# Kernel tuning notes

Measured on AMD Instinct MI355X. Metric: run time of the kernel, lower is better.

## Reference

```python
import math
import jax, jax.numpy as jnp
import numpy as np

B, T, D, H = 2, 2048, 1024, 16
N_LAYERS = 24


def get_slopes(n):
    def pow2(n):
        start = 2 ** (-2 ** (-(math.log2(n) - 3)))
        return [start * start ** i for i in range(n)]
    if math.log2(n).is_integer():
        return pow2(n)
    c = 2 ** math.floor(math.log2(n))
    return pow2(c) + get_slopes(2 * c)[0::2][: n - c]


def setup_inputs() -> dict:
    key = jax.random.key(0)
    ks = jax.random.split(key, 5)
    x = jax.random.normal(ks[0], (B, T, D), dtype=jnp.float32)
    Wq = 0.02 * jax.random.normal(ks[1], (D, D), dtype=jnp.float32)
    Wk = 0.02 * jax.random.normal(ks[2], (D, D), dtype=jnp.float32)
    Wv = 0.02 * jax.random.normal(ks[3], (D, D), dtype=jnp.float32)
    Wo = (0.02 / math.sqrt(2 * N_LAYERS)) * jax.random.normal(ks[4], (D, D), dtype=jnp.float32)
    z = jnp.zeros((D,), dtype=jnp.float32)
    return {"x": x, "Wq": Wq, "bq": z, "Wk": Wk, "bk": z, "Wv": Wv, "bv": z, "Wo": Wo, "bo": z}


def reference(x, Wq, bq, Wk, bk, Wv, bv, Wo, bo):
    Bb, Tt, C = x.shape
    hd = C // H
    # QKV projections -> (B, H, T, hd)
    q = (x @ Wq + bq).reshape(Bb, Tt, H, hd).transpose(0, 2, 1, 3)
    k = (x @ Wk + bk).reshape(Bb, Tt, H, hd).transpose(0, 2, 1, 3)
    v = (x @ Wv + bv).reshape(Bb, Tt, H, hd).transpose(0, 2, 1, 3)
    # scaled dot-product scores (B, H, T, T)
    attn = jnp.einsum('bhqd,bhkd->bhqk', q, k) / jnp.sqrt(jnp.asarray(hd, x.dtype))
    # ALiBi bias: module uses only last row of the relative-position matrix,
    # broadcast over query positions: -slope_h * (T-1 - j), shape (1, H, 1, T)
    slopes = jnp.asarray(get_slopes(H), dtype=x.dtype)
    alibi = -slopes[None, :, None, None] * (Tt - 1 - jnp.arange(Tt, dtype=x.dtype))[None, None, None, :]
    attn = attn + alibi
    # causal mask
    causal = jnp.tril(jnp.ones((Tt, Tt), dtype=bool))[None, None, :, :]
    attn = jnp.where(causal, attn, jnp.finfo(x.dtype).min)
    p = jax.nn.softmax(attn, axis=-1)
    out = jnp.einsum('bhqk,bhkd->bqhd', p, v).reshape(Bb, Tt, C)
    return out @ Wo + bo
```

## Files before the change

kernel.cpp:

```cpp
#include <hip/hip_runtime.h>
#include <hip/hip_bf16.h>

#define Bn 2
#define Tdim 2048
#define Ddim 1024
#define Hn 16
#define HD 64

typedef unsigned short u16;
typedef unsigned int u32;
typedef __attribute__((ext_vector_type(8))) __bf16 bf16x8;
typedef __attribute__((ext_vector_type(4))) float f32x4;
typedef __attribute__((ext_vector_type(16))) float f32x16;
typedef __attribute__((ext_vector_type(4))) u32 u32x4;

struct alignas(8) U16x4 { u16 x, y, z, w; };

__device__ __forceinline__ u16 f2bf(float f) {
  union { float f; u32 i; } v; v.f = f;
  u32 x = v.i;
  u32 r = (x + 0x7fffu + ((x >> 16) & 1u)) >> 16;
  return (u16)r;
}
__device__ __forceinline__ float bf2f(u16 u) {
  union { u32 i; float f; } v; v.i = ((u32)u) << 16; return v.f;
}
__device__ __forceinline__ u32 fbits(float f) {
  union { float f; u32 i; } v; v.f = f; return v.i;
}

__device__ __forceinline__ void cp16(const u16* g, u16* l) {
  __builtin_amdgcn_global_load_lds(
      (const __attribute__((address_space(1))) u32*)g,
      (__attribute__((address_space(3))) u32*)l, 16, 0, 0);
}

__device__ __forceinline__ f32x4 mfma16(bf16x8 a, bf16x8 b, f32x4 c) {
  return __builtin_amdgcn_mfma_f32_16x16x32_bf16(a, b, c, 0, 0, 0);
}
__device__ __forceinline__ f32x16 mfma32(bf16x8 a, bf16x8 b, f32x16 c) {
  return __builtin_amdgcn_mfma_f32_32x32x16_bf16(a, b, c, 0, 0, 0);
}

__global__ __launch_bounds__(256) void convert_x(const float* __restrict__ src,
                                                 u16* __restrict__ dst) {
  const int i = (blockIdx.x * 256 + threadIdx.x) * 8;
  u16 t[8];
#pragma unroll
  for (int j = 0; j < 8; j++) t[j] = f2bf(src[i + j]);
  *(bf16x8*)&dst[i] = *(const bf16x8*)t;
}

__global__ __launch_bounds__(256) void transpose_k(
    const float* __restrict__ s0, const float* __restrict__ s1,
    const float* __restrict__ s2, const float* __restrict__ s3,
    u16* __restrict__ dst) {
  const float* src = (blockIdx.z == 0) ? s0 : (blockIdx.z == 1) ? s1
                   : (blockIdx.z == 2) ? s2 : s3;
  u16* d = dst + (size_t)blockIdx.z * Ddim * Ddim;
  __shared__ u16 tile[32][33];
  const int tx = threadIdx.x, ty = threadIdx.y;
  const int x = blockIdx.x * 32 + tx;
  const int y0 = blockIdx.y * 32;
#pragma unroll
  for (int j = 0; j < 32; j += 8) tile[ty + j][tx] = f2bf(src[(size_t)(y0 + ty + j) * Ddim + x]);
  __syncthreads();
  const int xo = blockIdx.y * 32 + tx;
  const int yo0 = blockIdx.x * 32;
#pragma unroll
  for (int j = 0; j < 32; j += 8) d[(size_t)(yo0 + ty + j) * Ddim + xo] = tile[tx][ty + j];
}

__global__ __launch_bounds__(256, 2) void gemm_qkv(
    const u16* __restrict__ Xb, const u16* __restrict__ WT,
    const float* __restrict__ bq, const float* __restrict__ bk, const float* __restrict__ bv,
    u16* __restrict__ Q, u16* __restrict__ K, u16* __restrict__ Vt) {
  const int z = blockIdx.z;
  const u16* Wt = WT + (size_t)z * Ddim * Ddim;
  const float* bias = (z == 0) ? bq : (z == 1) ? bk : bv;
  u16* QK = (z == 0) ? Q : K;

  __shared__ alignas(16) u16 Alds[128 * 32];
  __shared__ alignas(16) u16 Blds[128 * 32];
  const int tid = threadIdx.x;
  const int w = tid >> 6, lane = tid & 63, ln = lane & 15, quad = lane >> 4;
  const int wm = (w >> 1) * 64, wn = (w & 1) * 64;
  const int tm = blockIdx.x * 128, tn = blockIdx.y * 128;

  f32x4 acc[4][4] = {};

  const int srow = tid >> 2, scol = (tid & 3) * 8;
  const u16* ag = Xb + (size_t)(tm + srow) * Ddim + scol;
  const u16* ag2 = ag + (size_t)64 * Ddim;
  const u16* bg = Wt + (size_t)(tn + srow) * Ddim + scol;
  const u16* bg2 = bg + (size_t)64 * Ddim;
  u16* al = &Alds[w * 512];
  u16* al2 = &Alds[2048 + w * 512];
  u16* bl = &Blds[w * 512];
  u16* bl2 = &Blds[2048 + w * 512];

  for (int k0 = 0; k0 < Ddim; k0 += 32) {
    __syncthreads();
    cp16(ag + k0, al);
    cp16(ag2 + k0, al2);
    cp16(bg + k0, bl);
    cp16(bg2 + k0, bl2);
    __syncthreads();
    bf16x8 af[4], bfr[4];
#pragma unroll
    for (int i = 0; i < 4; i++)
      af[i] = *(const bf16x8*)&Alds[(wm + i * 16 + ln) * 32 + quad * 8];
#pragma unroll
    for (int i = 0; i < 4; i++)
      bfr[i] = *(const bf16x8*)&Blds[(wn + i * 16 + ln) * 32 + quad * 8];
#pragma unroll
    for (int mi = 0; mi < 4; mi++)
#pragma unroll
      for (int ni = 0; ni < 4; ni++)
        acc[mi][ni] = mfma16(af[mi], bfr[ni], acc[mi][ni]);
  }

#pragma unroll
  for (int mi = 0; mi < 4; mi++) {
#pragma unroll
    for (int ni = 0; ni < 4; ni++) {
      const int gm0 = tm + wm + mi * 16 + quad * 4;
      const int gn = tn + wn + ni * 16 + ln;
      const float bv_ = bias[gn];
      const int hh = gn >> 6, dd = gn & 63;
      const int b0 = gm0 >> 11, t0 = gm0 & 2047;
      if (z < 2) {
        u16* p = QK + (((size_t)(b0 * Hn + hh) * Tdim) + t0) * HD + dd;
#pragma unroll
        for (int r = 0; r < 4; r++) p[r * HD] = f2bf(acc[mi][ni][r] + bv_);
      } else {
        U16x4 pk;
        pk.x = f2bf(acc[mi][ni][0] + bv_);
        pk.y = f2bf(acc[mi][ni][1] + bv_);
        pk.z = f2bf(acc[mi][ni][2] + bv_);
        pk.w = f2bf(acc[mi][ni][3] + bv_);
        *(U16x4*)&Vt[((size_t)(b0 * Hn + hh) * HD + dd) * Tdim + t0] = pk;
      }
    }
  }
}

#define KSTR 68
#define VSTR 132
#define L2E 1.44269504088896f
__global__ __launch_bounds__(256, 2) void attn_k(
    const u16* __restrict__ Q, const u16* __restrict__ K, const u16* __restrict__ Vt,
    u16* __restrict__ Op, float* __restrict__ lp) {
  __shared__ alignas(16) u16 Klds[128 * KSTR];
  __shared__ alignas(16) u16 Vtlds[64 * VSTR];

  const int bx = blockIdx.x;
  const int qb = 15 - (bx >> 1);
  const int s = bx & 1;
  const int bh = blockIdx.y;
  const int q0 = qb * 128;
  const int tid = threadIdx.x;
  const int w = tid >> 6, lane = tid & 63;
  const int qi = lane & 31, hf = lane >> 5;

  const u16* Qh = Q + (size_t)bh * Tdim * HD;
  const u16* Kh = K + (size_t)bh * Tdim * HD;
  const u16* Vh = Vt + (size_t)bh * HD * Tdim;
  const float slope = exp2f(-0.5f * (float)((bh & 15) + 1));

  const int nkt = qb + 1;
  const int h0 = (nkt + 1) >> 1;
  const int kt0 = s ? h0 : 0;
  const int kt1 = s ? nkt : h0;

  const int tg = q0 + w * 32 + qi;
  const float sl2 = slope * L2E;
  const float c1 = 0.125f * L2E;
  const float tt2 = (slope * (float)tg + 3.0f) * L2E;
  const float f4hf = (float)(4 * hf);
  float sg8[4], slm[4];
#pragma unroll
  for (int g = 0; g < 4; g++) sg8[g] = sl2 * (float)(8 * g);
#pragma unroll
  for (int m = 0; m < 4; m++) slm[m] = sl2 * (float)m;

  bf16x8 qf[4];
#pragma unroll
  for (int kc = 0; kc < 4; kc++)
    qf[kc] = *(const bf16x8*)&Qh[(size_t)tg * HD + kc * 16 + hf * 8];

  float lsum = 0.f;
  f32x16 oacc[2] = {};

  bf16x8 kreg[4], vreg[4];
  {
    const int kb = kt0 * 128;
#pragma unroll
    for (int c = 0; c < 4; c++) {
      const int e = c * 2048 + tid * 8;
      kreg[c] = *(const bf16x8*)&Kh[(size_t)(kb + (e >> 6)) * HD + (e & 63)];
      vreg[c] = *(const bf16x8*)&Vh[(size_t)(e >> 7) * Tdim + kb + (e & 127)];
    }
  }

  for (int kt = kt0; kt < kt1; kt++) {
    const int kb = kt * 128;
    __syncthreads();
#pragma unroll
    for (int c = 0; c < 4; c++) {
      const int e = c * 2048 + tid * 8;
      *(bf16x8*)&Klds[(e >> 6) * KSTR + (e & 63)] = kreg[c];
      *(bf16x8*)&Vtlds[(e >> 7) * VSTR + (e & 127)] = vreg[c];
    }
    __syncthreads();

    if (kt + 1 < kt1) {
      const int kb2 = kb + 128;
#pragma unroll
      for (int c = 0; c < 4; c++) {
        const int e = c * 2048 + tid * 8;
        kreg[c] = *(const bf16x8*)&Kh[(size_t)(kb2 + (e >> 6)) * HD + (e & 63)];
        vreg[c] = *(const bf16x8*)&Vh[(size_t)(e >> 7) * Tdim + kb2 + (e & 127)];
      }
    }

    f32x16 st[4] = {};
#pragma unroll
    for (int kc = 0; kc < 4; kc++) {
#pragma unroll
      for (int ni = 0; ni < 4; ni++) {
        bf16x8 kf = *(const bf16x8*)&Klds[(ni * 32 + qi) * KSTR + kc * 16 + hf * 8];
        st[ni] = mfma32(kf, qf[kc], st[ni]);
      }
    }

    const bool diag = (kt == nkt - 1);
    const float fkb = (float)kb + f4hf;
    bf16x8 pfrag[8];
#pragma unroll
    for (int ni = 0; ni < 4; ni++) {
      const float cni = __builtin_fmaf(sl2, fkb + (float)(32 * ni), -tt2);
      u32 pu[16];
      if (!diag) {
#pragma unroll
        for (int ri = 0; ri < 16; ri++) {
          const float e = __builtin_fmaf(st[ni][ri], c1, cni + sg8[ri >> 2] + slm[ri & 3]);
          const float p = __builtin_amdgcn_exp2f(e);
          lsum += p;
          pu[ri] = fbits(p) + 0x8000u;
        }
      } else {
#pragma unroll
        for (int ri = 0; ri < 16; ri++) {
          const int n = kb + ni * 32 + (ri & 3) + 8 * (ri >> 2) + 4 * hf;
          const float e = __builtin_fmaf(st[ni][ri], c1, cni + sg8[ri >> 2] + slm[ri & 3]);
          float p = __builtin_amdgcn_exp2f(e);
          if (n > tg) p = 0.f;
          lsum += p;
          pu[ri] = fbits(p) + 0x8000u;
        }
      }
      u32 pk[4][2];
#pragma unroll
      for (int g = 0; g < 4; g++) {
        pk[g][0] = __builtin_amdgcn_perm(pu[g * 4 + 1], pu[g * 4 + 0], 0x07060302u);
        pk[g][1] = __builtin_amdgcn_perm(pu[g * 4 + 3], pu[g * 4 + 2], 0x07060302u);
      }
#pragma unroll
      for (int a = 0; a < 2; a++) {
        const u32 snd0 = (hf == 0) ? pk[2 * a + 1][0] : pk[2 * a][0];
        const u32 snd1 = (hf == 0) ? pk[2 * a + 1][1] : pk[2 * a][1];
        const u32 rcv0 = (u32)__shfl_xor((int)snd0, 32);
        const u32 rcv1 = (u32)__shfl_xor((int)snd1, 32);
        u32x4 fr;
        fr.x = (hf == 0) ? pk[2 * a][0] : rcv0;
        fr.y = (hf == 0) ? pk[2 * a][1] : rcv1;
        fr.z = (hf == 0) ? rcv0 : pk[2 * a + 1][0];
        fr.w = (hf == 0) ? rcv1 : pk[2 * a + 1][1];
        pfrag[ni * 2 + a] = *(bf16x8*)&fr;
      }
    }

#pragma unroll
    for (int kf16 = 0; kf16 < 8; kf16++) {
#pragma unroll
      for (int nd = 0; nd < 2; nd++) {
        bf16x8 vf = *(const bf16x8*)&Vtlds[(nd * 32 + qi) * VSTR + kf16 * 16 + hf * 8];
        oacc[nd] = mfma32(pfrag[kf16], vf, oacc[nd]);
      }
    }
  }

  lsum += __shfl_xor(lsum, 32);
  if (hf == 0) lp[(size_t)s * 65536 + bh * Tdim + tg] = lsum;

  u16* Ob = Op + (size_t)s * (32u * Tdim * HD) + ((size_t)bh * Tdim) * HD;
#pragma unroll
  for (int nd = 0; nd < 2; nd++) {
#pragma unroll
    for (int ri = 0; ri < 16; ri++) {
      const int rq = (ri & 3) + 8 * (ri >> 2) + 4 * hf;
      const int t = q0 + w * 32 + rq;
      Ob[(size_t)t * HD + nd * 32 + qi] = f2bf(oacc[nd][ri]);
    }
  }
}

__global__ __launch_bounds__(256) void merge_k(const u16* __restrict__ Op,
                                               const float* __restrict__ lp,
                                               u16* __restrict__ AO) {
  const int i = blockIdx.x * 256 + threadIdx.x;
  const int d8 = i & 7;
  const int t = (i >> 3) & 2047;
  const int bh = i >> 14;
  const int b = bh >> 4, h = bh & 15;
  const float l = lp[bh * Tdim + t] + lp[65536 + bh * Tdim + t];
  const float inv = 1.0f / l;
  const size_t off = ((size_t)bh * Tdim + t) * HD + d8 * 8;
  const u16* O0 = Op + off;
  const u16* O1 = Op + (size_t)32 * Tdim * HD + off;
  u16 outv[8];
#pragma unroll
  for (int j = 0; j < 8; j++)
    outv[j] = f2bf((bf2f(O0[j]) + bf2f(O1[j])) * inv);
  *(bf16x8*)&AO[((size_t)(b * Tdim + t)) * Ddim + h * HD + d8 * 8] = *(const bf16x8*)outv;
}

__global__ __launch_bounds__(256, 2) void gemm_out(
    const u16* __restrict__ A, const u16* __restrict__ WoT, const float* __restrict__ bo,
    float* __restrict__ C) {
  __shared__ alignas(16) u16 Alds[128 * 32];
  __shared__ alignas(16) u16 Blds[128 * 32];
  const int tid = threadIdx.x;
  const int w = tid >> 6, lane = tid & 63, ln = lane & 15, quad = lane >> 4;
  const int wm = (w >> 1) * 64, wn = (w & 1) * 64;
  const int tm = blockIdx.x * 128, tn = blockIdx.y * 128;

  f32x4 acc[4][4] = {};

  const int srow = tid >> 2, scol = (tid & 3) * 8;
  const u16* ag = A + (size_t)(tm + srow) * Ddim + scol;
  const u16* ag2 = ag + (size_t)64 * Ddim;
  const u16* bg = WoT + (size_t)(tn + srow) * Ddim + scol;
  const u16* bg2 = bg + (size_t)64 * Ddim;
  u16* al = &Alds[w * 512];
  u16* al2 = &Alds[2048 + w * 512];
  u16* bl = &Blds[w * 512];
  u16* bl2 = &Blds[2048 + w * 512];

  for (int k0 = 0; k0 < Ddim; k0 += 32) {
    __syncthreads();
    cp16(ag + k0, al);
    cp16(ag2 + k0, al2);
    cp16(bg + k0, bl);
    cp16(bg2 + k0, bl2);
    __syncthreads();
    bf16x8 af[4], bfr[4];
#pragma unroll
    for (int i = 0; i < 4; i++)
      af[i] = *(const bf16x8*)&Alds[(wm + i * 16 + ln) * 32 + quad * 8];
#pragma unroll
    for (int i = 0; i < 4; i++)
      bfr[i] = *(const bf16x8*)&Blds[(wn + i * 16 + ln) * 32 + quad * 8];
#pragma unroll
    for (int mi = 0; mi < 4; mi++)
#pragma unroll
      for (int ni = 0; ni < 4; ni++)
        acc[mi][ni] = mfma16(af[mi], bfr[ni], acc[mi][ni]);
  }

#pragma unroll
  for (int mi = 0; mi < 4; mi++) {
#pragma unroll
    for (int ni = 0; ni < 4; ni++) {
      const int gm0 = tm + wm + mi * 16 + quad * 4;
      const int gn = tn + wn + ni * 16 + ln;
      const float bv_ = bo[gn];
#pragma unroll
      for (int r = 0; r < 4; r++)
        C[(size_t)(gm0 + r) * Ddim + gn] = acc[mi][ni][r] + bv_;
    }
  }
}

extern "C" void kernel_launch(void* const* d_in, const int* in_sizes, int n_in,
                              void* d_out, int out_size, void* d_ws, size_t ws_size,
                              hipStream_t stream) {
  (void)in_sizes; (void)n_in; (void)out_size; (void)ws_size;
  const float* x  = (const float*)d_in[0];
  const float* Wq = (const float*)d_in[1];
  const float* bq = (const float*)d_in[2];
  const float* Wk = (const float*)d_in[3];
  const float* bk = (const float*)d_in[4];
  const float* Wv = (const float*)d_in[5];
  const float* bv = (const float*)d_in[6];
  const float* Wo = (const float*)d_in[7];
  const float* bo = (const float*)d_in[8];

  char* ws = (char*)d_ws;
  const size_t MB = 1024 * 1024;
  u16* WT   = (u16*)(ws + 0 * MB);
  u16* Qb   = (u16*)(ws + 8 * MB);
  u16* Kb   = (u16*)(ws + 16 * MB);
  u16* Vtb  = (u16*)(ws + 24 * MB);
  u16* Xb   = (u16*)(ws + 32 * MB);
  u16* AO   = (u16*)(ws + 32 * MB);
  u16* Opart= (u16*)(ws + 40 * MB);
  float* lpart = (float*)(ws + 56 * MB);
  u16* WoT = WT + (size_t)3 * Ddim * Ddim;

  convert_x<<<dim3(2048), 256, 0, stream>>>(x, Xb);
  transpose_k<<<dim3(32, 32, 4), dim3(32, 8), 0, stream>>>(Wq, Wk, Wv, Wo, WT);

  gemm_qkv<<<dim3(32, 8, 3), 256, 0, stream>>>(Xb, WT, bq, bk, bv, Qb, Kb, Vtb);
  attn_k<<<dim3(32, 32), 256, 0, stream>>>(Qb, Kb, Vtb, Opart, lpart);
  merge_k<<<dim3(2048), 256, 0, stream>>>(Opart, lpart, AO);
  gemm_out<<<dim3(32, 8), 256, 0, stream>>>(AO, WoT, bo, (float*)d_out);
}
```

Baseline: 205.1 us.

## Pair causal query blocks per workgroup for balanced attention work

Each attention workgroup now handles two query blocks (p and 15-p), so every block does about the same amount of causal key work and the grid shrinks by half. The K/V prefetch continues across the segment boundary. The change also converts P to bf16 with v_cvt_pk_bf16_f32 instead of manual rounding and a perm, splits the row-sum accumulator in two, and raises wave priority around the MFMA loops. The risks are fewer workgroups (512 instead of 1024) and therefore less latency hiding, plus higher register pressure.

```diff
diff --git a/kernel.cpp b/kernel.cpp
--- a/kernel.cpp
+++ b/kernel.cpp
@@ -25,8 +25,11 @@
 __device__ __forceinline__ float bf2f(u16 u) {
   union { u32 i; float f; } v; v.i = ((u32)u) << 16; return v.f;
 }
-__device__ __forceinline__ u32 fbits(float f) {
-  union { float f; u32 i; } v; v.f = f; return v.i;
+
+__device__ __forceinline__ u32 cvtpk_bf16(float a, float b) {
+  u32 d;
+  asm("v_cvt_pk_bf16_f32 %0, %1, %2" : "=v"(d) : "v"(a), "v"(b));
+  return d;
 }
 
 __device__ __forceinline__ void cp16(const u16* g, u16* l) {
@@ -155,10 +158,9 @@
   __shared__ alignas(16) u16 Vtlds[64 * VSTR];
 
   const int bx = blockIdx.x;
-  const int qb = 15 - (bx >> 1);
+  const int p = bx >> 1;
   const int s = bx & 1;
   const int bh = blockIdx.y;
-  const int q0 = qb * 128;
   const int tid = threadIdx.x;
   const int w = tid >> 6, lane = tid & 63;
   const int qi = lane & 31, hf = lane >> 5;
@@ -168,15 +170,8 @@
   const u16* Vh = Vt + (size_t)bh * HD * Tdim;
   const float slope = exp2f(-0.5f * (float)((bh & 15) + 1));
 
-  const int nkt = qb + 1;
-  const int h0 = (nkt + 1) >> 1;
-  const int kt0 = s ? h0 : 0;
-  const int kt1 = s ? nkt : h0;
-
-  const int tg = q0 + w * 32 + qi;
   const float sl2 = slope * L2E;
   const float c1 = 0.125f * L2E;
-  const float tt2 = (slope * (float)tg + 3.0f) * L2E;
   const float f4hf = (float)(4 * hf);
   float sg8[4], slm[4];
 #pragma unroll
@@ -184,17 +179,19 @@
 #pragma unroll
   for (int m = 0; m < 4; m++) slm[m] = sl2 * (float)m;
 
-  bf16x8 qf[4];
-#pragma unroll
-  for (int kc = 0; kc < 4; kc++)
-    qf[kc] = *(const bf16x8*)&Qh[(size_t)tg * HD + kc * 16 + hf * 8];
-
-  float lsum = 0.f;
-  f32x16 oacc[2] = {};
+  const int qbs[2] = {p, 15 - p};
+  int K0[2], K1[2];
+#pragma unroll
+  for (int seg = 0; seg < 2; seg++) {
+    const int nk = qbs[seg] + 1;
+    const int h0 = (nk + 1) >> 1;
+    K0[seg] = s ? h0 : 0;
+    K1[seg] = s ? nk : h0;
+  }
 
   bf16x8 kreg[4], vreg[4];
   {
-    const int kb = kt0 * 128;
+    const int kb = ((K0[0] < K1[0]) ? K0[0] : K0[1]) * 128;
 #pragma unroll
     for (int c = 0; c < 4; c++) {
       const int e = c * 2048 + tid * 8;
@@ -203,105 +200,130 @@
     }
   }
 
-  for (int kt = kt0; kt < kt1; kt++) {
-    const int kb = kt * 128;
-    __syncthreads();
-#pragma unroll
-    for (int c = 0; c < 4; c++) {
-      const int e = c * 2048 + tid * 8;
-      *(bf16x8*)&Klds[(e >> 6) * KSTR + (e & 63)] = kreg[c];
-      *(bf16x8*)&Vtlds[(e >> 7) * VSTR + (e & 127)] = vreg[c];
-    }
-    __syncthreads();
-
-    if (kt + 1 < kt1) {
-      const int kb2 = kb + 128;
+  for (int seg = 0; seg < 2; seg++) {
+    const int qb = qbs[seg];
+    const int kt0 = K0[seg], kt1 = K1[seg];
+    const int nkt = qb + 1;
+    const int q0 = qb * 128;
+    const int tg = q0 + w * 32 + qi;
+    const float tt2 = (slope * (float)tg + 3.0f) * L2E;
+
+    bf16x8 qf[4];
+#pragma unroll
+    for (int kc = 0; kc < 4; kc++)
+      qf[kc] = *(const bf16x8*)&Qh[(size_t)tg * HD + kc * 16 + hf * 8];
+
+    float ls0 = 0.f, ls1 = 0.f;
+    f32x16 oacc[2] = {};
+
+    for (int kt = kt0; kt < kt1; kt++) {
+      const int kb = kt * 128;
+      __syncthreads();
 #pragma unroll
       for (int c = 0; c < 4; c++) {
         const int e = c * 2048 + tid * 8;
-        kreg[c] = *(const bf16x8*)&Kh[(size_t)(kb2 + (e >> 6)) * HD + (e & 63)];
-        vreg[c] = *(const bf16x8*)&Vh[(size_t)(e >> 7) * Tdim + kb2 + (e & 127)];
-      }
+        *(bf16x8*)&Klds[(e >> 6) * KSTR + (e & 63)] = kreg[c];
+        *(bf16x8*)&Vtlds[(e >> 7) * VSTR + (e & 127)] = vreg[c];
+      }
+      __syncthreads();
+
+      {
+        const int nxt = (kt + 1 < kt1) ? (kt + 1) : ((seg == 0) ? K0[1] : -1);
+        if (nxt >= 0) {
+          const int kb2 = nxt * 128;
+#pragma unroll
+          for (int c = 0; c < 4; c++) {
+            const int e = c * 2048 + tid * 8;
+            kreg[c] = *(const bf16x8*)&Kh[(size_t)(kb2 + (e >> 6)) * HD + (e & 63)];
+            vreg[c] = *(const bf16x8*)&Vh[(size_t)(e >> 7) * Tdim + kb2 + (e & 127)];
+          }
+        }
+      }
+
+      f32x16 st[4] = {};
+      __builtin_amdgcn_s_setprio(1);
+#pragma unroll
+      for (int kc = 0; kc < 4; kc++) {
+#pragma unroll
+        for (int ni = 0; ni < 4; ni++) {
+          bf16x8 kf = *(const bf16x8*)&Klds[(ni * 32 + qi) * KSTR + kc * 16 + hf * 8];
+          st[ni] = mfma32(kf, qf[kc], st[ni]);
+        }
+      }
+      __builtin_amdgcn_s_setprio(0);
+
+      const bool diag = (kt == nkt - 1);
+      const float fkb = (float)kb + f4hf;
+      bf16x8 pfrag[8];
+#pragma unroll
+      for (int ni = 0; ni < 4; ni++) {
+        const float cni = __builtin_fmaf(sl2, fkb + (float)(32 * ni), -tt2);
+        float pv[16];
+        if (!diag) {
+#pragma unroll
+          for (int ri = 0; ri < 16; ri++) {
+            const float e = __builtin_fmaf(st[ni][ri], c1, cni + sg8[ri >> 2] + slm[ri & 3]);
+            const float pp = __builtin_amdgcn_exp2f(e);
+            if (ri & 1) ls1 += pp; else ls0 += pp;
+            pv[ri] = pp;
+          }
+        } else {
+#pragma unroll
+          for (int ri = 0; ri < 16; ri++) {
+            const int n = kb + ni * 32 + (ri & 3) + 8 * (ri >> 2) + 4 * hf;
+            const float e = __builtin_fmaf(st[ni][ri], c1, cni + sg8[ri >> 2] + slm[ri & 3]);
+            float pp = __builtin_amdgcn_exp2f(e);
+            if (n > tg) pp = 0.f;
+            if (ri & 1) ls1 += pp; else ls0 += pp;
+            pv[ri] = pp;
+          }
+        }
+        u32 pk[4][2];
+#pragma unroll
+        for (int g = 0; g < 4; g++) {
+          pk[g][0] = cvtpk_bf16(pv[g * 4 + 0], pv[g * 4 + 1]);
+          pk[g][1] = cvtpk_bf16(pv[g * 4 + 2], pv[g * 4 + 3]);
+        }
+#pragma unroll
+        for (int a = 0; a < 2; a++) {
+          const u32 snd0 = (hf == 0) ? pk[2 * a + 1][0] : pk[2 * a][0];
+          const u32 snd1 = (hf == 0) ? pk[2 * a + 1][1] : pk[2 * a][1];
+          const u32 rcv0 = (u32)__shfl_xor((int)snd0, 32);
+          const u32 rcv1 = (u32)__shfl_xor((int)snd1, 32);
+          u32x4 fr;
+          fr.x = (hf == 0) ? pk[2 * a][0] : rcv0;
+          fr.y = (hf == 0) ? pk[2 * a][1] : rcv1;
+          fr.z = (hf == 0) ? rcv0 : pk[2 * a + 1][0];
+          fr.w = (hf == 0) ? rcv1 : pk[2 * a + 1][1];
+          pfrag[ni * 2 + a] = *(bf16x8*)&fr;
+        }
+      }
+
+      __builtin_amdgcn_s_setprio(1);
+#pragma unroll
+      for (int kf16 = 0; kf16 < 8; kf16++) {
+#pragma unroll
+        for (int nd = 0; nd < 2; nd++) {
+          bf16x8 vf = *(const bf16x8*)&Vtlds[(nd * 32 + qi) * VSTR + kf16 * 16 + hf * 8];
+          oacc[nd] = mfma32(pfrag[kf16], vf, oacc[nd]);
+        }
+      }
+      __builtin_amdgcn_s_setprio(0);
     }
 
-    f32x16 st[4] = {};
-#pragma unroll
-    for (int kc = 0; kc < 4; kc++) {
-#pragma unroll
-      for (int ni = 0; ni < 4; ni++) {
-        bf16x8 kf = *(const bf16x8*)&Klds[(ni * 32 + qi) * KSTR + kc * 16 + hf * 8];
-        st[ni] = mfma32(kf, qf[kc], st[ni]);
-      }
-    }
-
-    const bool diag = (kt == nkt - 1);
-    const float fkb = (float)kb + f4hf;
-    bf16x8 pfrag[8];
-#pragma unroll
-    for (int ni = 0; ni < 4; ni++) {
-      const float cni = __builtin_fmaf(sl2, fkb + (float)(32 * ni), -tt2);
-      u32 pu[16];
-      if (!diag) {
-#pragma unroll
-        for (int ri = 0; ri < 16; ri++) {
-          const float e = __builtin_fmaf(st[ni][ri], c1, cni + sg8[ri >> 2] + slm[ri & 3]);
-          const float p = __builtin_amdgcn_exp2f(e);
-          lsum += p;
-          pu[ri] = fbits(p) + 0x8000u;
-        }
-      } else {
-#pragma unroll
-        for (int ri = 0; ri < 16; ri++) {
-          const int n = kb + ni * 32 + (ri & 3) + 8 * (ri >> 2) + 4 * hf;
-          const float e = __builtin_fmaf(st[ni][ri], c1, cni + sg8[ri >> 2] + slm[ri & 3]);
-          float p = __builtin_amdgcn_exp2f(e);
-          if (n > tg) p = 0.f;
-          lsum += p;
-          pu[ri] = fbits(p) + 0x8000u;
-        }
-      }
-      u32 pk[4][2];
-#pragma unroll
-      for (int g = 0; g < 4; g++) {
-        pk[g][0] = __builtin_amdgcn_perm(pu[g * 4 + 1], pu[g * 4 + 0], 0x07060302u);
-        pk[g][1] = __builtin_amdgcn_perm(pu[g * 4 + 3], pu[g * 4 + 2], 0x07060302u);
-      }
-#pragma unroll
-      for (int a = 0; a < 2; a++) {
-        const u32 snd0 = (hf == 0) ? pk[2 * a + 1][0] : pk[2 * a][0];
-        const u32 snd1 = (hf == 0) ? pk[2 * a + 1][1] : pk[2 * a][1];
-        const u32 rcv0 = (u32)__shfl_xor((int)snd0, 32);
-        const u32 rcv1 = (u32)__shfl_xor((int)snd1, 32);
-        u32x4 fr;
-        fr.x = (hf == 0) ? pk[2 * a][0] : rcv0;
-        fr.y = (hf == 0) ? pk[2 * a][1] : rcv1;
-        fr.z = (hf == 0) ? rcv0 : pk[2 * a + 1][0];
-        fr.w = (hf == 0) ? rcv1 : pk[2 * a + 1][1];
-        pfrag[ni * 2 + a] = *(bf16x8*)&fr;
-      }
-    }
-
-#pragma unroll
-    for (int kf16 = 0; kf16 < 8; kf16++) {
-#pragma unroll
-      for (int nd = 0; nd < 2; nd++) {
-        bf16x8 vf = *(const bf16x8*)&Vtlds[(nd * 32 + qi) * VSTR + kf16 * 16 + hf * 8];
-        oacc[nd] = mfma32(pfrag[kf16], vf, oacc[nd]);
-      }
-    }
-  }
-
-  lsum += __shfl_xor(lsum, 32);
-  if (hf == 0) lp[(size_t)s * 65536 + bh * Tdim + tg] = lsum;
-
-  u16* Ob = Op + (size_t)s * (32u * Tdim * HD) + ((size_t)bh * Tdim) * HD;
-#pragma unroll
-  for (int nd = 0; nd < 2; nd++) {
-#pragma unroll
-    for (int ri = 0; ri < 16; ri++) {
-      const int rq = (ri & 3) + 8 * (ri >> 2) + 4 * hf;
-      const int t = q0 + w * 32 + rq;
-      Ob[(size_t)t * HD + nd * 32 + qi] = f2bf(oacc[nd][ri]);
+    float lsum = ls0 + ls1;
+    lsum += __shfl_xor(lsum, 32);
+    if (hf == 0) lp[(size_t)s * 65536 + bh * Tdim + tg] = lsum;
+
+    u16* Ob = Op + (size_t)s * (32u * Tdim * HD) + ((size_t)bh * Tdim) * HD;
+#pragma unroll
+    for (int nd = 0; nd < 2; nd++) {
+#pragma unroll
+      for (int ri = 0; ri < 16; ri++) {
+        const int rq = (ri & 3) + 8 * (ri >> 2) + 4 * hf;
+        const int t = q0 + w * 32 + rq;
+        Ob[(size_t)t * HD + nd * 32 + qi] = f2bf(oacc[nd][ri]);
+      }
     }
   }
 }
@@ -413,7 +435,7 @@
   transpose_k<<<dim3(32, 32, 4), dim3(32, 8), 0, stream>>>(Wq, Wk, Wv, Wo, WT);
 
   gemm_qkv<<<dim3(32, 8, 3), 256, 0, stream>>>(Xb, WT, bq, bk, bv, Qb, Kb, Vtb);
-  attn_k<<<dim3(32, 32), 256, 0, stream>>>(Qb, Kb, Vtb, Opart, lpart);
+  attn_k<<<dim3(16, 32), 256, 0, stream>>>(Qb, Kb, Vtb, Opart, lpart);
   merge_k<<<dim3(2048), 256, 0, stream>>>(Opart, lpart, AO);
   gemm_out<<<dim3(32, 8), 256, 0, stream>>>(AO, WoT, bo, (float*)d_out);
 }
```

Result: faster. 190.5 us (-7.1%).
